# Optimization experiments

Hardware: AMD Instinct MI355X
Metric: run time of the kernel (lower is better)

## Reference

```python
import jax, jax.numpy as jnp
import numpy as np
from jax import lax

DDELTA = 0.001
COEFF = 1.0 / (4.0 * DDELTA)  # 250.0
PAD = 1


def _conv(x, w):
    # x: [B,Cin,H,W], w: [Cout,Cin,kh,kw] -> [B,Cout,H,W] (same padding)
    return lax.conv_general_dilated(x, w, (1, 1), [(PAD, PAD), (PAD, PAD)],
                                    dimension_numbers=("NCHW", "OIHW", "NCHW"))


def _cconv(xr, xi, wr, wi, br, bi):
    # complex conv: (xr + i xi) * (wr + i wi) + (br + i bi)
    yr = _conv(xr, wr) - _conv(xi, wi) + br[None, :, None, None]
    yi = _conv(xr, wi) + _conv(xi, wr) + bi[None, :, None, None]
    return yr, yi


def _sigma(x):
    # smooth ReLU: relu outside |x|<=ddelta, quadratic blend inside
    return jnp.where(jnp.abs(x) > DDELTA,
                     jax.nn.relu(x),
                     x * x * COEFF + 0.5 * x + 0.25 * DDELTA)


def setup_inputs() -> dict:
    key = jax.random.key(0)
    ks = jax.random.split(key, 16)
    B, F, H, W = 2, 48, 320, 320
    d = {
        "x_real": jax.random.normal(ks[0], (B, 1, H, W), jnp.float32),
        "x_imag": jax.random.normal(ks[1], (B, 1, H, W), jnp.float32),
        "w0_real": jax.random.normal(ks[2], (F, 1, 3, 3), jnp.float32) * 0.2,
        "w0_imag": jax.random.normal(ks[3], (F, 1, 3, 3), jnp.float32) * 0.2,
        "b0_real": jax.random.normal(ks[4], (F,), jnp.float32) * 0.05,
        "b0_imag": jax.random.normal(ks[5], (F,), jnp.float32) * 0.05,
        "w1_real": jax.random.normal(ks[6], (F, F, 3, 3), jnp.float32) * 0.05,
        "w1_imag": jax.random.normal(ks[7], (F, F, 3, 3), jnp.float32) * 0.05,
        "b1_real": jax.random.normal(ks[8], (F,), jnp.float32) * 0.05,
        "b1_imag": jax.random.normal(ks[9], (F,), jnp.float32) * 0.05,
        "w2_real": jax.random.normal(ks[10], (F, F, 3, 3), jnp.float32) * 0.05,
        "w2_imag": jax.random.normal(ks[11], (F, F, 3, 3), jnp.float32) * 0.05,
        "b2_real": jax.random.normal(ks[12], (F,), jnp.float32) * 0.05,
        "b2_imag": jax.random.normal(ks[13], (F,), jnp.float32) * 0.05,
    }
    return d


def reference(x_real, x_imag,
              w0_real, w0_imag, b0_real, b0_imag,
              w1_real, w1_imag, b1_real, b1_imag,
              w2_real, w2_imag, b2_real, b2_imag):
    # layer 0: conv only (no activation before first conv)
    r, i = _cconv(x_real, x_imag, w0_real, w0_imag, b0_real, b0_imag)
    cache = [(r, i)]
    for (wr, wi, br, bi) in ((w1_real, w1_imag, b1_real, b1_imag),
                             (w2_real, w2_imag, b2_real, b2_imag)):
        ar, ai = _sigma(r), _sigma(i)  # activation applied separately to real/imag
        r, i = _cconv(ar, ai, wr, wi, br, bi)
        cache.append((r, i))
    # cache list of complex tensors -> stacked real repr [n_convs, B, F, H, W, 2]
    return jnp.stack([jnp.stack([cr, ci], axis=-1) for cr, ci in cache], axis=0)
```

## Files before the change

kernel.cpp:

```cpp
#include <hip/hip_runtime.h>

typedef __attribute__((ext_vector_type(8))) short short8;
typedef __attribute__((ext_vector_type(4))) float f32x4;

#define IMG_H 320
#define IMG_W 320
#define NBATCH 2
#define NFEAT 48
#define PLANE (IMG_H * IMG_W)
#define KDIM 864
#define NDIM 96

#define TH 8
#define TW 32
#define FI 4
#define BLK 512
#define HALO_H (TH + 2)
#define HALO_W (TW + 2)
#define HALO_PIX (HALO_H * HALO_W)
#define CPAD 104
#define NCHUNK 12
#define STAGE_TOT (HALO_PIX * NCHUNK)
#define TS 260

__device__ __forceinline__ float sigma_f(float x) {
    float ax = __builtin_fabsf(x);
    float quad = x * x * 250.0f + 0.5f * x + 0.00025f;
    float rel = fmaxf(x, 0.0f);
    return ax > 0.001f ? rel : quad;
}

__device__ __forceinline__ unsigned short f2bf(float f) {
    union { float f; unsigned u; } v; v.f = f;
    unsigned r = (v.u + 0x7FFFu + ((v.u >> 16) & 1u)) >> 16;
    return (unsigned short)r;
}

__global__ void wprep_kernel(const float* __restrict__ wr1, const float* __restrict__ wi1,
                             const float* __restrict__ wr2, const float* __restrict__ wi2,
                             unsigned short* __restrict__ wt1, unsigned short* __restrict__ wt2) {
    int idx = blockIdx.x * 256 + threadIdx.x;
    if (idx >= 2 * NDIM * KDIM) return;
    int which = idx >= NDIM * KDIM;
    int id = which ? idx - NDIM * KDIM : idx;
    const float* wr = which ? wr2 : wr1;
    const float* wi = which ? wi2 : wi1;
    unsigned short* wt = which ? wt2 : wt1;
    int n = id / KDIM;
    int k = id - n * KDIM;
    int tap = k / 96;
    int cp = k - tap * 96;
    int f = (n < 48) ? n : n - 48;
    int c = (cp < 48) ? cp : cp - 48;
    int widx = (f * 48 + c) * 9 + tap;
    float v;
    if (n < 48) v = (cp < 48) ?  wr[widx] : -wi[widx];
    else        v = (cp < 48) ?  wi[widx] :  wr[widx];
    wt[id] = f2bf(v);
}

template<int OUT_NHWC>
__global__ __launch_bounds__(256) void layer0_kernel(
    const float* __restrict__ xr, const float* __restrict__ xi,
    const float* __restrict__ wr, const float* __restrict__ wi,
    const float* __restrict__ br, const float* __restrict__ bi,
    float* __restrict__ out, unsigned short* __restrict__ nhwc) {
    int idx = blockIdx.x * 256 + threadIdx.x;
    int b = idx / PLANE;
    int p = idx - b * PLANE;
    int h = p / IMG_W;
    int w = p - h * IMG_W;
    const float* xrp = xr + (size_t)b * PLANE;
    const float* xip = xi + (size_t)b * PLANE;

    float ar[9], ai[9];
#pragma unroll
    for (int dy = 0; dy < 3; ++dy) {
#pragma unroll
        for (int dx = 0; dx < 3; ++dx) {
            int hh = h + dy - 1, ww = w + dx - 1;
            bool ok = ((unsigned)hh < (unsigned)IMG_H) && ((unsigned)ww < (unsigned)IMG_W);
            ar[dy * 3 + dx] = ok ? xrp[hh * IMG_W + ww] : 0.0f;
            ai[dy * 3 + dx] = ok ? xip[hh * IMG_W + ww] : 0.0f;
        }
    }

    short8 nh[12];
#pragma unroll
    for (int f = 0; f < NFEAT; ++f) {
        float yr = br[f], yi = bi[f];
#pragma unroll
        for (int t = 0; t < 9; ++t) {
            float wrv = wr[f * 9 + t], wiv = wi[f * 9 + t];
            yr += ar[t] * wrv - ai[t] * wiv;
            yi += ar[t] * wiv + ai[t] * wrv;
        }
        float2 o; o.x = yr; o.y = yi;
        *reinterpret_cast<float2*>(out + ((size_t)(b * NFEAT + f) * PLANE + p) * 2) = o;
        if (OUT_NHWC) {
            nh[f >> 3][f & 7] = (short)f2bf(sigma_f(yr));
            nh[6 + (f >> 3)][f & 7] = (short)f2bf(sigma_f(yi));
        }
    }
    if (OUT_NHWC) {
        unsigned short* dst = nhwc + (size_t)(b * PLANE + p) * 96;
#pragma unroll
        for (int c = 0; c < 12; ++c)
            *reinterpret_cast<short8*>(dst + c * 8) = nh[c];
    }
}

template<int IN_MODE, int OUT_NHWC>
__global__ __launch_bounds__(BLK, 4) void cconv_kernel(
    const float* __restrict__ inF, const unsigned short* __restrict__ inH,
    const unsigned short* __restrict__ wt,
    const float* __restrict__ br, const float* __restrict__ bi,
    float* __restrict__ outF, unsigned short* __restrict__ outH) {
    __shared__ __align__(16) unsigned short tile[HALO_PIX * CPAD];

    int bid0 = blockIdx.x;
    int bid = (bid0 & 7) * 100 + (bid0 >> 3);
    int wblk = bid % (IMG_W / TW);
    int t = bid / (IMG_W / TW);
    int hblk = t % (IMG_H / TH);
    int b = t / (IMG_H / TH);
    int h0 = hblk * TH, w0 = wblk * TW;

    int tid = threadIdx.x;

    if (IN_MODE == 1) {
        const unsigned short* inHb = inH + (size_t)b * PLANE * 96;
        short8 v[8];
        int dst[8];
#pragma unroll
        for (int s = 0; s < 8; ++s) {
            int it = tid + s * BLK;
            int pix = it / NCHUNK;
            int chunk = it - pix * NCHUNK;
            int hh = pix / HALO_W;
            int ww = pix - hh * HALO_W;
            int h = h0 + hh - 1, w = w0 + ww - 1;
            bool inimg = ((unsigned)h < (unsigned)IMG_H) && ((unsigned)w < (unsigned)IMG_W);
            bool live = it < STAGE_TOT;
            dst[s] = live ? (pix * CPAD + chunk * 8) : -1;
            if (live && inimg)
                v[s] = *reinterpret_cast<const short8*>(
                    inHb + ((size_t)(h * IMG_W + w) * 96 + chunk * 8));
            else
                v[s] = (short8){0, 0, 0, 0, 0, 0, 0, 0};
        }
#pragma unroll
        for (int s = 0; s < 8; ++s)
            if (dst[s] >= 0) *reinterpret_cast<short8*>(&tile[dst[s]]) = v[s];
    } else {
        const float* inFb = inF + (size_t)b * NFEAT * PLANE * 2;
        for (int it = tid; it < STAGE_TOT; it += BLK) {
            int pix = it / NCHUNK;
            int chunk = it - pix * NCHUNK;
            int hh = pix / HALO_W;
            int ww = pix - hh * HALO_W;
            int h = h0 + hh - 1, w = w0 + ww - 1;
            bool ok = ((unsigned)h < (unsigned)IMG_H) && ((unsigned)w < (unsigned)IMG_W);
            int c0 = chunk * 8;
            short8 v;
#pragma unroll
            for (int j = 0; j < 8; ++j) {
                int cp = c0 + j;
                int c = (cp < 48) ? cp : cp - 48;
                int ri = (cp < 48) ? 0 : 1;
                float x = ok ? inFb[((size_t)c * PLANE + h * IMG_W + w) * 2 + ri] : 0.0f;
                v[j] = (short)f2bf(sigma_f(x));
            }
            *reinterpret_cast<short8*>(&tile[pix * CPAD + chunk * 8]) = v;
        }
    }
    __syncthreads();

    int wave = tid >> 6, lane = tid & 63;
    int wm = wave >> 1, wn = wave & 1;
    int lrow = lane & 15, lk = lane >> 4;

    int basepix[FI];
#pragma unroll
    for (int fi = 0; fi < FI; ++fi) {
        int m = wm * (FI * 16) + fi * 16 + lrow;
        basepix[fi] = (m >> 5) * HALO_W + (m & 31);
    }

    const unsigned short* wrow[3];
#pragma unroll
    for (int nf = 0; nf < 3; ++nf)
        wrow[nf] = wt + (size_t)(wn * 48 + nf * 16 + lrow) * KDIM + lk * 8;

    f32x4 acc[FI][3];
#pragma unroll
    for (int fi = 0; fi < FI; ++fi)
#pragma unroll
        for (int nf = 0; nf < 3; ++nf)
            acc[fi][nf] = (f32x4){0.f, 0.f, 0.f, 0.f};

    short8 bf[2][3];
#pragma unroll
    for (int nf = 0; nf < 3; ++nf)
        bf[0][nf] = *reinterpret_cast<const short8*>(wrow[nf]);

#pragma unroll
    for (int it = 0; it < 27; ++it) {
        const int cur = it & 1;
        const int tap = it / 3, cb = it - tap * 3;
        if (it < 26) {
            const int it2 = it + 1;
            const int tap2 = it2 / 3, cb2 = it2 - tap2 * 3;
#pragma unroll
            for (int nf = 0; nf < 3; ++nf)
                bf[cur ^ 1][nf] = *reinterpret_cast<const short8*>(wrow[nf] + tap2 * 96 + cb2 * 32);
        }
        const int tapoff = (tap / 3) * HALO_W + (tap % 3);
#pragma unroll
        for (int fi = 0; fi < FI; ++fi) {
            short8 a = *reinterpret_cast<const short8*>(
                &tile[(basepix[fi] + tapoff) * CPAD + cb * 32 + lk * 8]);
#pragma unroll
            for (int nf = 0; nf < 3; ++nf)
                acc[fi][nf] = __builtin_amdgcn_mfma_f32_16x16x32_bf16(a, bf[cur][nf], acc[fi][nf], 0, 0, 0);
        }
    }

#pragma unroll
    for (int nf = 0; nf < 3; ++nf) {
        int f = nf * 16 + lrow;
        float bias = wn ? bi[f] : br[f];
#pragma unroll
        for (int fi = 0; fi < FI; ++fi)
#pragma unroll
            for (int j = 0; j < 4; ++j)
                acc[fi][nf][j] += bias;
    }

    float* tf = reinterpret_cast<float*>(tile);
    int fl = tid >> 5;
    int p0 = tid & 31;
    __syncthreads();

#pragma unroll
    for (int r = 0; r < 3; ++r) {
        if (OUT_NHWC) {
            int n = wn * 48 + r * 16 + lrow;
#pragma unroll
            for (int fi = 0; fi < FI; ++fi) {
#pragma unroll
                for (int j = 0; j < 4; ++j) {
                    int m = wm * (FI * 16) + fi * 16 + lk * 4 + j;
                    int h = h0 + (m >> 5), w = w0 + (m & 31);
                    outH[(size_t)(b * PLANE + h * IMG_W + w) * 96 + n] =
                        f2bf(sigma_f(acc[fi][r][j]));
                }
            }
        }
        int np = wn * 16 + lrow;
#pragma unroll
        for (int fi = 0; fi < FI; ++fi)
            *reinterpret_cast<f32x4*>(&tf[np * TS + wm * (FI * 16) + fi * 16 + lk * 4]) = acc[fi][r];
        __syncthreads();
        float* obase = outF + (((size_t)(b * NFEAT + r * 16 + fl) * IMG_H + h0) * IMG_W + w0) * 2;
#pragma unroll
        for (int g = 0; g < TH; ++g) {
            float2 o;
            o.x = tf[fl * TS + g * 32 + p0];
            o.y = tf[(16 + fl) * TS + g * 32 + p0];
            *reinterpret_cast<float2*>(obase + ((size_t)g * IMG_W + p0) * 2) = o;
        }
        if (r < 2) __syncthreads();
    }
}

extern "C" void kernel_launch(void* const* d_in, const int* in_sizes, int n_in,
                              void* d_out, int out_size, void* d_ws, size_t ws_size,
                              hipStream_t stream) {
    const float* x_real  = (const float*)d_in[0];
    const float* x_imag  = (const float*)d_in[1];
    const float* w0_real = (const float*)d_in[2];
    const float* w0_imag = (const float*)d_in[3];
    const float* b0_real = (const float*)d_in[4];
    const float* b0_imag = (const float*)d_in[5];
    const float* w1_real = (const float*)d_in[6];
    const float* w1_imag = (const float*)d_in[7];
    const float* b1_real = (const float*)d_in[8];
    const float* b1_imag = (const float*)d_in[9];
    const float* w2_real = (const float*)d_in[10];
    const float* w2_imag = (const float*)d_in[11];
    const float* b2_real = (const float*)d_in[12];
    const float* b2_imag = (const float*)d_in[13];

    float* out = (float*)d_out;
    unsigned short* wt1 = (unsigned short*)d_ws;
    unsigned short* wt2 = wt1 + NDIM * KDIM;

    const size_t wt_bytes = (size_t)2 * NDIM * KDIM * 2;
    const size_t nhwc_elems = (size_t)NBATCH * PLANE * 96;
    const size_t need = wt_bytes + 2 * nhwc_elems * 2;
    const bool fast = ws_size >= need;

    unsigned short* nhwc0 = (unsigned short*)((char*)d_ws + wt_bytes);
    unsigned short* nhwc1 = nhwc0 + nhwc_elems;

    const size_t layer_sz = (size_t)NBATCH * NFEAT * PLANE * 2;

    wprep_kernel<<<(2 * NDIM * KDIM + 255) / 256, 256, 0, stream>>>(
        w1_real, w1_imag, w2_real, w2_imag, wt1, wt2);

    const int l0_grid = NBATCH * PLANE / 256;
    const int conv_grid = NBATCH * (IMG_H / TH) * (IMG_W / TW);

    if (fast) {
        layer0_kernel<1><<<l0_grid, 256, 0, stream>>>(
            x_real, x_imag, w0_real, w0_imag, b0_real, b0_imag, out, nhwc0);
        cconv_kernel<1, 1><<<conv_grid, BLK, 0, stream>>>(
            nullptr, nhwc0, wt1, b1_real, b1_imag, out + layer_sz, nhwc1);
        cconv_kernel<1, 0><<<conv_grid, BLK, 0, stream>>>(
            nullptr, nhwc1, wt2, b2_real, b2_imag, out + 2 * layer_sz, nullptr);
    } else {
        layer0_kernel<0><<<l0_grid, 256, 0, stream>>>(
            x_real, x_imag, w0_real, w0_imag, b0_real, b0_imag, out, nullptr);
        cconv_kernel<0, 0><<<conv_grid, BLK, 0, stream>>>(
            out, nullptr, wt1, b1_real, b1_imag, out + layer_sz, nullptr);
        cconv_kernel<0, 0><<<conv_grid, BLK, 0, stream>>>(
            out + layer_sz, nullptr, wt2, b2_real, b2_imag, out + 2 * layer_sz, nullptr);
    }
}
```

Baseline: 176.3 us.

## Switch conv MFMA to 32x32x16 tiles with XOR-swizzled LDS and vectorized epilogue

Replaces the 16x16x32 bf16 MFMA tiling (4 M-frags x 3 N-frags per wave) with 32x32x16 MFMAs where each wave owns one 32-pixel row and all 96 output channels. The staged input tile gets an XOR swizzle on 8-channel chunks to cut LDS bank conflicts. The epilogue is restructured into two halves that write full channel rows to LDS, then emit coalesced float2 stores and 16-byte NHWC bf16 stores instead of scalar short stores. This cuts A-operand LDS reads and scattered global writes, at the cost of a longer dependent MFMA chain per wave and larger accumulator registers.

```diff
diff --git a/kernel.cpp b/kernel.cpp
--- a/kernel.cpp
+++ b/kernel.cpp
@@ -2,6 +2,7 @@
 
 typedef __attribute__((ext_vector_type(8))) short short8;
 typedef __attribute__((ext_vector_type(4))) float f32x4;
+typedef __attribute__((ext_vector_type(16))) float f32x16;
 
 #define IMG_H 320
 #define IMG_W 320
@@ -13,7 +14,6 @@
 
 #define TH 8
 #define TW 32
-#define FI 4
 #define BLK 512
 #define HALO_H (TH + 2)
 #define HALO_W (TW + 2)
@@ -21,7 +21,7 @@
 #define CPAD 104
 #define NCHUNK 12
 #define STAGE_TOT (HALO_PIX * NCHUNK)
-#define TS 260
+#define EPAD 100
 
 __device__ __forceinline__ float sigma_f(float x) {
     float ax = __builtin_fabsf(x);
@@ -142,7 +142,8 @@
             int h = h0 + hh - 1, w = w0 + ww - 1;
             bool inimg = ((unsigned)h < (unsigned)IMG_H) && ((unsigned)w < (unsigned)IMG_W);
             bool live = it < STAGE_TOT;
-            dst[s] = live ? (pix * CPAD + chunk * 8) : -1;
+            int sc = chunk ^ ((pix >> 3) & 3);
+            dst[s] = live ? (pix * CPAD + sc * 8) : -1;
             if (live && inimg)
                 v[s] = *reinterpret_cast<const short8*>(
                     inHb + ((size_t)(h * IMG_W + w) * 96 + chunk * 8));
@@ -171,106 +172,104 @@
                 float x = ok ? inFb[((size_t)c * PLANE + h * IMG_W + w) * 2 + ri] : 0.0f;
                 v[j] = (short)f2bf(sigma_f(x));
             }
-            *reinterpret_cast<short8*>(&tile[pix * CPAD + chunk * 8]) = v;
+            int sc = chunk ^ ((pix >> 3) & 3);
+            *reinterpret_cast<short8*>(&tile[pix * CPAD + sc * 8]) = v;
         }
     }
     __syncthreads();
 
     int wave = tid >> 6, lane = tid & 63;
-    int wm = wave >> 1, wn = wave & 1;
-    int lrow = lane & 15, lk = lane >> 4;
-
-    int basepix[FI];
-#pragma unroll
-    for (int fi = 0; fi < FI; ++fi) {
-        int m = wm * (FI * 16) + fi * 16 + lrow;
-        basepix[fi] = (m >> 5) * HALO_W + (m & 31);
-    }
+    int l31 = lane & 31, lk5 = lane >> 5;
+    int base = wave * HALO_W + l31;
 
     const unsigned short* wrow[3];
 #pragma unroll
-    for (int nf = 0; nf < 3; ++nf)
-        wrow[nf] = wt + (size_t)(wn * 48 + nf * 16 + lrow) * KDIM + lk * 8;
-
-    f32x4 acc[FI][3];
-#pragma unroll
-    for (int fi = 0; fi < FI; ++fi)
-#pragma unroll
-        for (int nf = 0; nf < 3; ++nf)
-            acc[fi][nf] = (f32x4){0.f, 0.f, 0.f, 0.f};
+    for (int g = 0; g < 3; ++g)
+        wrow[g] = wt + (size_t)(g * 32 + l31) * KDIM + lk5 * 8;
+
+    f32x16 acc[3];
+#pragma unroll
+    for (int g = 0; g < 3; ++g)
+#pragma unroll
+        for (int r = 0; r < 16; ++r) acc[g][r] = 0.0f;
 
     short8 bf[2][3];
 #pragma unroll
-    for (int nf = 0; nf < 3; ++nf)
-        bf[0][nf] = *reinterpret_cast<const short8*>(wrow[nf]);
-
-#pragma unroll
-    for (int it = 0; it < 27; ++it) {
+    for (int g = 0; g < 3; ++g)
+        bf[0][g] = *reinterpret_cast<const short8*>(wrow[g]);
+
+#pragma unroll
+    for (int it = 0; it < 54; ++it) {
         const int cur = it & 1;
-        const int tap = it / 3, cb = it - tap * 3;
-        if (it < 26) {
+        const int tap = it / 6, ks = it - tap * 6;
+        if (it < 53) {
             const int it2 = it + 1;
-            const int tap2 = it2 / 3, cb2 = it2 - tap2 * 3;
-#pragma unroll
-            for (int nf = 0; nf < 3; ++nf)
-                bf[cur ^ 1][nf] = *reinterpret_cast<const short8*>(wrow[nf] + tap2 * 96 + cb2 * 32);
-        }
-        const int tapoff = (tap / 3) * HALO_W + (tap % 3);
-#pragma unroll
-        for (int fi = 0; fi < FI; ++fi) {
-            short8 a = *reinterpret_cast<const short8*>(
-                &tile[(basepix[fi] + tapoff) * CPAD + cb * 32 + lk * 8]);
-#pragma unroll
-            for (int nf = 0; nf < 3; ++nf)
-                acc[fi][nf] = __builtin_amdgcn_mfma_f32_16x16x32_bf16(a, bf[cur][nf], acc[fi][nf], 0, 0, 0);
-        }
-    }
-
-#pragma unroll
-    for (int nf = 0; nf < 3; ++nf) {
-        int f = nf * 16 + lrow;
-        float bias = wn ? bi[f] : br[f];
-#pragma unroll
-        for (int fi = 0; fi < FI; ++fi)
-#pragma unroll
-            for (int j = 0; j < 4; ++j)
-                acc[fi][nf][j] += bias;
+            const int tap2 = it2 / 6, ks2 = it2 - tap2 * 6;
+#pragma unroll
+            for (int g = 0; g < 3; ++g)
+                bf[cur ^ 1][g] = *reinterpret_cast<const short8*>(wrow[g] + tap2 * 96 + ks2 * 16);
+        }
+        const int p = base + (tap / 3) * HALO_W + (tap % 3);
+        const int c16 = (ks * 2 + lk5) ^ ((p >> 3) & 3);
+        short8 a = *reinterpret_cast<const short8*>(&tile[p * CPAD + c16 * 8]);
+#pragma unroll
+        for (int g = 0; g < 3; ++g)
+            acc[g] = __builtin_amdgcn_mfma_f32_32x32x16_bf16(a, bf[cur][g], acc[g], 0, 0, 0);
+    }
+
+#pragma unroll
+    for (int g = 0; g < 3; ++g) {
+        int n = g * 32 + l31;
+        float bias = (n < NFEAT) ? br[n] : bi[n - NFEAT];
+#pragma unroll
+        for (int r = 0; r < 16; ++r) acc[g][r] += bias;
     }
 
     float* tf = reinterpret_cast<float*>(tile);
-    int fl = tid >> 5;
-    int p0 = tid & 31;
     __syncthreads();
 
 #pragma unroll
-    for (int r = 0; r < 3; ++r) {
+    for (int half = 0; half < 2; ++half) {
+        if ((wave >> 2) == half) {
+            int rl = wave & 3;
+#pragma unroll
+            for (int g = 0; g < 3; ++g)
+#pragma unroll
+                for (int r = 0; r < 16; ++r) {
+                    int m = (r & 3) + 8 * (r >> 2) + 4 * lk5;
+                    tf[(rl * 32 + m) * EPAD + g * 32 + l31] = acc[g][r];
+                }
+        }
+        __syncthreads();
+#pragma unroll
+        for (int j = 0; j < 12; ++j) {
+            int idx = j * BLK + tid;
+            int f = idx >> 7;
+            int pl = idx & 127;
+            float2 o;
+            o.x = tf[pl * EPAD + f];
+            o.y = tf[pl * EPAD + NFEAT + f];
+            int h = h0 + half * 4 + (pl >> 5);
+            int w = w0 + (pl & 31);
+            *reinterpret_cast<float2*>(outF + (((size_t)(b * NFEAT + f) * IMG_H + h) * IMG_W + w) * 2) = o;
+        }
         if (OUT_NHWC) {
-            int n = wn * 48 + r * 16 + lrow;
-#pragma unroll
-            for (int fi = 0; fi < FI; ++fi) {
-#pragma unroll
-                for (int j = 0; j < 4; ++j) {
-                    int m = wm * (FI * 16) + fi * 16 + lk * 4 + j;
-                    int h = h0 + (m >> 5), w = w0 + (m & 31);
-                    outH[(size_t)(b * PLANE + h * IMG_W + w) * 96 + n] =
-                        f2bf(sigma_f(acc[fi][r][j]));
-                }
+#pragma unroll
+            for (int jj = 0; jj < 3; ++jj) {
+                int idx = jj * BLK + tid;
+                int pl = idx / 12;
+                int chunk = idx - pl * 12;
+                const float* src = &tf[pl * EPAD + chunk * 8];
+                short8 v;
+#pragma unroll
+                for (int u = 0; u < 8; ++u) v[u] = (short)f2bf(sigma_f(src[u]));
+                int h = h0 + half * 4 + (pl >> 5);
+                int w = w0 + (pl & 31);
+                *reinterpret_cast<short8*>(
+                    outH + ((size_t)(b * PLANE + h * IMG_W + w) * 96 + chunk * 8)) = v;
             }
         }
-        int np = wn * 16 + lrow;
-#pragma unroll
-        for (int fi = 0; fi < FI; ++fi)
-            *reinterpret_cast<f32x4*>(&tf[np * TS + wm * (FI * 16) + fi * 16 + lk * 4]) = acc[fi][r];
-        __syncthreads();
-        float* obase = outF + (((size_t)(b * NFEAT + r * 16 + fl) * IMG_H + h0) * IMG_W + w0) * 2;
-#pragma unroll
-        for (int g = 0; g < TH; ++g) {
-            float2 o;
-            o.x = tf[fl * TS + g * 32 + p0];
-            o.y = tf[(16 + fl) * TS + g * 32 + p0];
-            *reinterpret_cast<float2*>(obase + ((size_t)g * IMG_W + p0) * 2) = o;
-        }
-        if (r < 2) __syncthreads();
+        if (half == 0) __syncthreads();
     }
 }
 
```

Result: slower. 245.7 us (+39.3%).
